# Optimization experiments

Hardware: AMD Instinct MI355X
Metric: run time of the kernel (lower is better)

The kernel has to match this reference:

```python
import jax, jax.numpy as jnp
import numpy as np
import math

EMBED_DIM = 2048
NUM_HEADS = 16
D_K = 128
BSZ = 2
SEQ = 2048


def make_freq_pos_enc(dim, max_seq_len):
    # inv_freq over dim/2 freqs, then interleave-repeat each freq twice: (f r), r=2
    inv_freq = 1.0 / (10000.0 ** (jnp.arange(0, dim, 2, dtype=jnp.float32) / dim))
    pos = jnp.arange(max_seq_len, dtype=jnp.float32)
    pe = jnp.einsum('p,f->pf', pos, inv_freq)                 # [S, dim/2]
    return jnp.repeat(pe, 2, axis=-1)                          # [S, dim], pattern (f r)


def rotate_half(u):
    # pairs are interleaved: (..., d r) with r=2
    u = u.reshape(*u.shape[:-1], -1, 2)
    u1, u2 = u[..., 0], u[..., 1]
    return jnp.stack((-u2, u1), axis=-1).reshape(*u.shape[:-2], -1)


def rotate(u, pos_enc):
    pe = pos_enc[: u.shape[-2]]                                # [S, d_k]
    return u * jnp.cos(pe) + rotate_half(u) * jnp.sin(pe)


def setup_inputs() -> dict:
    key = jax.random.key(0)
    ks = jax.random.split(key, 5)
    scale = 1.0 / math.sqrt(EMBED_DIM)
    return {
        'x': jax.random.normal(ks[0], (BSZ, SEQ, EMBED_DIM), dtype=jnp.float32),
        'wq': jax.random.normal(ks[1], (NUM_HEADS * D_K, EMBED_DIM), dtype=jnp.float32) * scale,
        'wk': jax.random.normal(ks[2], (NUM_HEADS * D_K, EMBED_DIM), dtype=jnp.float32) * scale,
        'wv': jax.random.normal(ks[3], (NUM_HEADS * D_K, EMBED_DIM), dtype=jnp.float32) * scale,
        'wo': jax.random.normal(ks[4], (EMBED_DIM, NUM_HEADS * D_K), dtype=jnp.float32) * scale,
        'freq_pos_enc': make_freq_pos_enc(D_K, SEQ),
        'mask': jnp.zeros((SEQ, SEQ), dtype=jnp.float32),  # dead arg in original forward
        'num_heads': NUM_HEADS,
        'd_k': D_K,
    }


def reference(x, wq, wk, wv, wo, freq_pos_enc, mask, num_heads, d_k):
    bsz, seq_len, _ = x.shape
    # projections (nn.Linear, no bias): x @ W^T
    def proj(w):
        p = jnp.einsum('bse,de->bsd', x, w)
        return p.reshape(bsz, seq_len, num_heads, d_k).transpose(0, 2, 1, 3)  # [B,H,S,d]
    q, k, v = proj(wq), proj(wk), proj(wv)
    q, k = rotate(q, freq_pos_enc), rotate(k, freq_pos_enc)
    # regenerated causal mask (0 on/below diagonal, -inf above)
    causal = jnp.where(
        jnp.arange(seq_len)[:, None] >= jnp.arange(seq_len)[None, :],
        0.0, -jnp.inf).astype(x.dtype)
    scores = jnp.einsum('bhsd,bhtd->bhst', q, k) / math.sqrt(d_k) + causal
    weights = jax.nn.softmax(scores, axis=-1)
    attn = jnp.einsum('bhst,bhtd->bhsd', weights, v)           # [B,H,S,d]
    attn = attn.transpose(0, 2, 1, 3).reshape(bsz, seq_len, -1)
    return jnp.einsum('bsd,ed->bse', attn, wo)


if __name__ == '__main__':
    out = reference(**setup_inputs())
    print(out.shape, out.dtype)
```

## Files before the change

kernel.cpp:

```cpp
#include <hip/hip_runtime.h>


typedef unsigned short u16;
typedef unsigned int   u32;
typedef __attribute__((ext_vector_type(4)))  float f32x4;
typedef __attribute__((ext_vector_type(16))) float f32x16;
typedef __attribute__((ext_vector_type(8)))  short short8;
typedef __attribute__((ext_vector_type(4)))  u16   u16x4;
typedef __attribute__((ext_vector_type(2)))  u16   u16x2;

#define NB   2
#define NH   16
#define SEQ  2048
#define DK   128
#define EMB  2048

__device__ __forceinline__ u16 f2bf(float f) {
    union { float f; unsigned int u; } v; v.f = f;
    unsigned int r = v.u + 0x7FFFu + ((v.u >> 16) & 1u);
    return (u16)(r >> 16);
}
__device__ __forceinline__ float bf2f(u16 h) {
    union { unsigned int u; float f; } v; v.u = ((unsigned int)h) << 16;
    return v.f;
}
__device__ __forceinline__ f32x4 mfma16(short8 a, short8 b, f32x4 c) {
    return __builtin_amdgcn_mfma_f32_16x16x32_bf16(a, b, c, 0, 0, 0);
}
__device__ __forceinline__ f32x16 mfma32(short8 a, short8 b, f32x16 c) {
    return __builtin_amdgcn_mfma_f32_32x32x16_bf16(a, b, c, 0, 0, 0);
}

#define GLDS(gsrc, ldst) __builtin_amdgcn_global_load_lds( \
    (const __attribute__((address_space(1))) void*)(gsrc), \
    (__attribute__((address_space(3))) void*)(ldst), 16, 0, 0)

__global__ __launch_bounds__(256) void cast_f32_bf16(const float* __restrict__ in,
                                                     u16* __restrict__ out, int n4) {
    int i = blockIdx.x * 256 + threadIdx.x;
    if (i >= n4) return;
    f32x4 v = ((const f32x4*)in)[i];
    u16x4 o;
    o[0] = f2bf(v[0]); o[1] = f2bf(v[1]); o[2] = f2bf(v[2]); o[3] = f2bf(v[3]);
    ((u16x4*)out)[i] = o;
}

__global__ __launch_bounds__(256) void rope_table(const float* __restrict__ freq,
                                                  float* __restrict__ ct,
                                                  float* __restrict__ st) {
    int i = blockIdx.x * 256 + threadIdx.x;
    int s = i >> 6, d2 = i & 63;
    float pe = freq[s * DK + d2 * 2];
    ct[i] = cosf(pe);
    st[i] = sinf(pe);
}

__global__ __launch_bounds__(256) void rope_apply(u16* __restrict__ Qb, u16* __restrict__ Kb,
                                                  const float* __restrict__ ct,
                                                  const float* __restrict__ st) {
    int i = blockIdx.x * 256 + threadIdx.x;
    int d2 = i & 63;
    int s  = (i >> 6) & (SEQ - 1);
    float c  = ct[(s << 6) + d2];
    float sn = st[(s << 6) + d2];
    size_t off = (size_t)i * 2;
    u16x2 q = *(const u16x2*)(Qb + off);
    float q0 = bf2f(q[0]), q1 = bf2f(q[1]);
    u16x2 qo; qo[0] = f2bf(q0 * c - q1 * sn); qo[1] = f2bf(q1 * c + q0 * sn);
    *(u16x2*)(Qb + off) = qo;
    u16x2 k = *(const u16x2*)(Kb + off);
    float k0 = bf2f(k[0]), k1 = bf2f(k[1]);
    u16x2 ko; ko[0] = f2bf(k0 * c - k1 * sn); ko[1] = f2bf(k1 * c + k0 * sn);
    *(u16x2*)(Kb + off) = ko;
}

template <int MODE>
__global__ __launch_bounds__(256) void gemm_ring(const u16* __restrict__ A,
                                                 const u16* __restrict__ B,
                                                 void* __restrict__ Cout,
                                                 int M, int N, int K) {
    __shared__ __align__(16) u16 As[3 * 4096];
    __shared__ __align__(16) u16 Bs[3 * 4096];
    const int tid  = threadIdx.x;
    const int lane = tid & 63;
    const int wid  = tid >> 6;
    const int wm   = wid >> 1, wn = wid & 1;
    const int nwgx = (int)gridDim.x;
    const int wgid = (int)blockIdx.y * nwgx + (int)blockIdx.x;
    const int cpx  = (nwgx * (int)gridDim.y) >> 3;
    const int swz  = (wgid & 7) * cpx + (wgid >> 3);
    const int m0   = (swz % nwgx) * 128, n0 = (swz / nwgx) * 128;
    const int lr   = lane & 15, lk = lane >> 4;

    const u16* Asrc = A + (size_t)(m0 + (tid >> 2)) * K + (tid & 3) * 8;
    const u16* Bsrc = B + (size_t)(n0 + (tid >> 2)) * K + (tid & 3) * 8;
    const int  dst0 = wid * 512;

    f32x4 acc[4][4] = {};
    const int NT = K >> 5;

#pragma unroll
    for (int i = 0; i < 2; ++i) {
        GLDS(Asrc + (size_t)i * 64 * K,      &As[i * 2048 + dst0]);
        GLDS(Bsrc + (size_t)i * 64 * K,      &Bs[i * 2048 + dst0]);
    }
#pragma unroll
    for (int i = 0; i < 2; ++i) {
        GLDS(Asrc + (size_t)i * 64 * K + 32, &As[4096 + i * 2048 + dst0]);
        GLDS(Bsrc + (size_t)i * 64 * K + 32, &Bs[4096 + i * 2048 + dst0]);
    }

    int buf = 0;
    for (int t = 0; t < NT; ++t) {
        if (t < NT - 1) asm volatile("s_waitcnt vmcnt(4)" ::: "memory");
        else            asm volatile("s_waitcnt vmcnt(0)" ::: "memory");
        __builtin_amdgcn_s_barrier();

        short8 af[4], bf[4];
#pragma unroll
        for (int i = 0; i < 4; ++i)
            af[i] = *(const short8*)&As[buf * 4096 + (wm * 64 + i * 16 + lr) * 32 + lk * 8];
#pragma unroll
        for (int j = 0; j < 4; ++j)
            bf[j] = *(const short8*)&Bs[buf * 4096 + (wn * 64 + j * 16 + lr) * 32 + lk * 8];

        if (t + 2 < NT) {
            int b2 = buf + 2; if (b2 >= 3) b2 -= 3;
            const u16* a2  = Asrc + (size_t)(t + 2) * 32;
            const u16* b2p = Bsrc + (size_t)(t + 2) * 32;
#pragma unroll
            for (int i = 0; i < 2; ++i) {
                GLDS(a2  + (size_t)i * 64 * K, &As[b2 * 4096 + i * 2048 + dst0]);
                GLDS(b2p + (size_t)i * 64 * K, &Bs[b2 * 4096 + i * 2048 + dst0]);
            }
        }

        __builtin_amdgcn_s_setprio(1);
#pragma unroll
        for (int i = 0; i < 4; ++i)
#pragma unroll
            for (int j = 0; j < 4; ++j)
                acc[i][j] = mfma16(af[i], bf[j], acc[i][j]);
        __builtin_amdgcn_s_setprio(0);

        buf = (buf == 2) ? 0 : buf + 1;
    }

#pragma unroll
    for (int i = 0; i < 4; ++i) {
#pragma unroll
        for (int j = 0; j < 4; ++j) {
#pragma unroll
            for (int r = 0; r < 4; ++r) {
                int m = m0 + wm * 64 + i * 16 + lk * 4 + r;
                int n = n0 + wn * 64 + j * 16 + lr;
                float v = acc[i][j][r];
                if (MODE == 0) {
                    int b = m >> 11, s = m & (SEQ - 1), h = n >> 7, d = n & (DK - 1);
                    ((u16*)Cout)[(((size_t)(b * NH + h) * SEQ + s) * DK) + d] = f2bf(v);
                } else if (MODE == 1) {
                    int h = m >> 7, d = m & (DK - 1), b = n >> 11, s = n & (SEQ - 1);
                    ((u16*)Cout)[(((size_t)(b * NH + h) * DK + d) * SEQ) + s] = f2bf(v);
                } else {
                    ((float*)Cout)[(size_t)m * N + n] = v;
                }
            }
        }
    }
}

__global__ __launch_bounds__(64, 2) void attn32(const u16* __restrict__ Q,
                                                const u16* __restrict__ K,
                                                const u16* __restrict__ VT,
                                                u16* __restrict__ O) {
    const int gid  = blockIdx.x;
    const int bh   = (gid & 7) * 4 + ((gid >> 3) & 3);
    const int qc   = 63 - (gid >> 5);
    const int l    = threadIdx.x;
    const int q32  = l & 31;
    const int half = l >> 5;
    const int q0   = qc * 32;
    const int nt   = qc + 1;

    const u16* Qg  = Q  + ((size_t)bh * SEQ + q0) * DK;
    const u16* Kg  = K  + (size_t)bh * SEQ * DK;
    const u16* VTg = VT + (size_t)bh * DK * SEQ;

    short8 qf[8];
#pragma unroll
    for (int kq = 0; kq < 8; ++kq)
        qf[kq] = *(const short8*)(Qg + q32 * DK + kq * 16 + half * 8);

    f32x16 oacc[4] = {};
    float m = -INFINITY, lsum = 0.f;

    auto loadK = [&](short8 (&kf)[8], int t) {
#pragma unroll
        for (int kq = 0; kq < 8; ++kq)
            kf[kq] = *(const short8*)(Kg + (size_t)(t * 32 + q32) * DK + kq * 16 + half * 8);
    };
    auto loadV = [&](short8 (&vf)[8], int t) {
#pragma unroll
        for (int i = 0; i < 8; ++i) {
            int dblk = i >> 1, ch = i & 1;
            vf[i] = *(const short8*)(VTg + (size_t)(dblk * 32 + q32) * SEQ
                                     + t * 32 + ch * 16 + half * 8);
        }
    };
    auto compute = [&](short8 (&kf)[8], short8 (&vf)[8], bool diag) {
        const float rs = 0.08838834764831845f;
        f32x16 sacc = {};
#pragma unroll
        for (int kq = 0; kq < 8; ++kq) sacc = mfma32(kf[kq], qf[kq], sacc);
        float tmax = -INFINITY;
#pragma unroll
        for (int r = 0; r < 16; ++r) {
            int kk = (r & 3) + 8 * (r >> 2) + 4 * half;
            float s = sacc[r] * rs;
            if (diag && kk > q32) s = -INFINITY;
            sacc[r] = s;
            tmax = fmaxf(tmax, s);
        }
        tmax = fmaxf(tmax, __shfl_xor(tmax, 32));
        if (__any(tmax - m > 8.0f)) {
            float mn = fmaxf(m, tmax);
            float sc = __expf(m - mn);
            m = mn; lsum *= sc;
#pragma unroll
            for (int d = 0; d < 4; ++d)
#pragma unroll
                for (int r = 0; r < 16; ++r) oacc[d][r] *= sc;
        }
        float tsum = 0.f;
#pragma unroll
        for (int r = 0; r < 16; ++r) { sacc[r] = __expf(sacc[r] - m); tsum += sacc[r]; }
        tsum += __shfl_xor(tsum, 32);
        lsum += tsum;
        u32 pk[8];
#pragma unroll
        for (int i = 0; i < 8; ++i)
            pk[i] = ((u32)f2bf(sacc[2 * i + 1]) << 16) | (u32)f2bf(sacc[2 * i]);
        u32 s0 = __shfl_xor((int)pk[0], 32), s1 = __shfl_xor((int)pk[1], 32);
        u32 s2 = __shfl_xor((int)pk[2], 32), s3 = __shfl_xor((int)pk[3], 32);
        u32 s4 = __shfl_xor((int)pk[4], 32), s5 = __shfl_xor((int)pk[5], 32);
        u32 s6 = __shfl_xor((int)pk[6], 32), s7 = __shfl_xor((int)pk[7], 32);
        union { u32 wd[4]; short8 s8; } P0, P1;
        P0.wd[0] = half ? s2    : pk[0];  P0.wd[1] = half ? s3    : pk[1];
        P0.wd[2] = half ? pk[2] : s0;     P0.wd[3] = half ? pk[3] : s1;
        P1.wd[0] = half ? s6    : pk[4];  P1.wd[1] = half ? s7    : pk[5];
        P1.wd[2] = half ? pk[6] : s4;     P1.wd[3] = half ? pk[7] : s5;
#pragma unroll
        for (int d = 0; d < 4; ++d) {
            oacc[d] = mfma32(vf[2 * d],     P0.s8, oacc[d]);
            oacc[d] = mfma32(vf[2 * d + 1], P1.s8, oacc[d]);
        }
    };

    short8 kA[8], kB[8], vA[8], vB[8];
    loadK(kA, 0);
    loadV(vA, 0);
    int t = 0;
    while (true) {
        if (t + 1 < nt) { loadK(kB, t + 1); loadV(vB, t + 1); }
        compute(kA, vA, t == qc);
        if (++t >= nt) break;
        if (t + 1 < nt) { loadK(kA, t + 1); loadV(vA, t + 1); }
        compute(kB, vB, t == qc);
        if (++t >= nt) break;
    }

    float inv = 1.0f / lsum;
    const int b = bh >> 4, h = bh & 15;
    u16* Og = O + ((size_t)b * SEQ + q0 + q32) * EMB + h * DK;
#pragma unroll
    for (int d = 0; d < 4; ++d)
#pragma unroll
        for (int rq = 0; rq < 4; ++rq) {
            u16x4 o4;
#pragma unroll
            for (int j = 0; j < 4; ++j) o4[j] = f2bf(oacc[d][rq * 4 + j] * inv);
            *(u16x4*)(Og + d * 32 + rq * 8 + half * 4) = o4;
        }
}

extern "C" void kernel_launch(void* const* d_in, const int* in_sizes, int n_in,
                              void* d_out, int out_size, void* d_ws, size_t ws_size,
                              hipStream_t stream) {
    const float* x    = (const float*)d_in[0];
    const float* wq   = (const float*)d_in[1];
    const float* wk   = (const float*)d_in[2];
    const float* wv   = (const float*)d_in[3];
    const float* wo   = (const float*)d_in[4];
    const float* freq = (const float*)d_in[5];

    char* ws = (char*)d_ws;
    u16*  xb  = (u16*)(ws);
    u16*  wqb = (u16*)(ws + 16777216);
    u16*  wkb = (u16*)(ws + 25165824);
    u16*  wvb = (u16*)(ws + 33554432);
    u16*  wob = (u16*)(ws + 41943040);
    u16*  Qb  = (u16*)(ws + 50331648);
    u16*  Kb  = (u16*)(ws + 67108864);
    u16*  VTb = (u16*)(ws + 83886080);
    float* ct = (float*)(ws + 100663296);
    float* st = (float*)(ws + 101187584);
    u16*  attn = xb;

    cast_f32_bf16<<<8192, 256, 0, stream>>>(x,  xb,  2097152);
    cast_f32_bf16<<<4096, 256, 0, stream>>>(wq, wqb, 1048576);
    cast_f32_bf16<<<4096, 256, 0, stream>>>(wk, wkb, 1048576);
    cast_f32_bf16<<<4096, 256, 0, stream>>>(wv, wvb, 1048576);
    cast_f32_bf16<<<4096, 256, 0, stream>>>(wo, wob, 1048576);
    rope_table<<<512, 256, 0, stream>>>(freq, ct, st);

    gemm_ring<0><<<dim3(32, 16), 256, 0, stream>>>(xb,  wqb, Qb,  4096, 2048, 2048);
    gemm_ring<0><<<dim3(32, 16), 256, 0, stream>>>(xb,  wkb, Kb,  4096, 2048, 2048);
    gemm_ring<1><<<dim3(16, 32), 256, 0, stream>>>(wvb, xb,  VTb, 2048, 4096, 2048);

    rope_apply<<<16384, 256, 0, stream>>>(Qb, Kb, ct, st);

    attn32<<<2048, 64, 0, stream>>>(Qb, Kb, VTb, attn);

    gemm_ring<3><<<dim3(32, 16), 256, 0, stream>>>(attn, wob, d_out, 4096, 2048, 2048);
}
```

Before: 340.3 us.

## Stage K/V tiles through LDS with async copies and pair causal query chunks

The attention kernel now stages K and V^T tiles into double-buffered, XOR-swizzled shared memory with direct global-to-LDS loads and explicit vmcnt waits, replacing the per-lane register double buffering. Each block handles two query chunks (63-p and p), so causal work is balanced and the grid is halved. MFMA sections are wrapped in setprio. The intent is to cut register pressure and global load latency and to balance causal work. The cost is LDS traffic and fewer blocks in flight. It relies on a GLDS helper and hand-written waitcnt counts that must match the number of loads issued.

```diff
diff --git a/kernel.cpp b/kernel.cpp
--- a/kernel.cpp
+++ b/kernel.cpp
@@ -169,118 +169,143 @@
     }
 }
 
-__global__ __launch_bounds__(64, 2) void attn32(const u16* __restrict__ Q,
-                                                const u16* __restrict__ K,
-                                                const u16* __restrict__ VT,
-                                                u16* __restrict__ O) {
+__global__ __launch_bounds__(64, 2) void attn_lds(const u16* __restrict__ Q,
+                                                  const u16* __restrict__ K,
+                                                  const u16* __restrict__ VT,
+                                                  u16* __restrict__ O) {
     const int gid  = blockIdx.x;
     const int bh   = (gid & 7) * 4 + ((gid >> 3) & 3);
-    const int qc   = 63 - (gid >> 5);
+    const int p    = gid >> 5;
     const int l    = threadIdx.x;
     const int q32  = l & 31;
     const int half = l >> 5;
-    const int q0   = qc * 32;
-    const int nt   = qc + 1;
-
-    const u16* Qg  = Q  + ((size_t)bh * SEQ + q0) * DK;
+
+    __shared__ __align__(16) u16 Ksh[2][4096];
+    __shared__ __align__(16) u16 Vsh[2][4096];
+
     const u16* Kg  = K  + (size_t)bh * SEQ * DK;
     const u16* VTg = VT + (size_t)bh * DK * SEQ;
-
-    short8 qf[8];
-#pragma unroll
-    for (int kq = 0; kq < 8; ++kq)
-        qf[kq] = *(const short8*)(Qg + q32 * DK + kq * 16 + half * 8);
-
-    f32x16 oacc[4] = {};
-    float m = -INFINITY, lsum = 0.f;
-
-    auto loadK = [&](short8 (&kf)[8], int t) {
-#pragma unroll
-        for (int kq = 0; kq < 8; ++kq)
-            kf[kq] = *(const short8*)(Kg + (size_t)(t * 32 + q32) * DK + kq * 16 + half * 8);
-    };
-    auto loadV = [&](short8 (&vf)[8], int t) {
+    const int b = bh >> 4, h = bh & 15;
+
+    auto stage = [&](int t, int bufn) {
 #pragma unroll
         for (int i = 0; i < 8; ++i) {
-            int dblk = i >> 1, ch = i & 1;
-            vf[i] = *(const short8*)(VTg + (size_t)(dblk * 32 + q32) * SEQ
-                                     + t * 32 + ch * 16 + half * 8);
+            int cid = i * 64 + l;
+            int kr = cid >> 4, kc = cid & 15;
+            GLDS(Kg + (size_t)(t * 32 + kr) * DK + ((kc ^ (kr & 7)) * 8),
+                 &Ksh[bufn][i * 512]);
+            int vr = cid >> 2, vc = cid & 3;
+            GLDS(VTg + (size_t)vr * SEQ + t * 32 + ((vc ^ ((vr >> 1) & 3)) * 8),
+                 &Vsh[bufn][i * 512]);
         }
     };
-    auto compute = [&](short8 (&kf)[8], short8 (&vf)[8], bool diag) {
-        const float rs = 0.08838834764831845f;
-        f32x16 sacc = {};
-#pragma unroll
-        for (int kq = 0; kq < 8; ++kq) sacc = mfma32(kf[kq], qf[kq], sacc);
-        float tmax = -INFINITY;
-#pragma unroll
-        for (int r = 0; r < 16; ++r) {
-            int kk = (r & 3) + 8 * (r >> 2) + 4 * half;
-            float s = sacc[r] * rs;
-            if (diag && kk > q32) s = -INFINITY;
-            sacc[r] = s;
-            tmax = fmaxf(tmax, s);
+
+    auto process = [&](int qc) {
+        const int q0 = qc * 32;
+        const int nt = qc + 1;
+        const u16* Qg = Q + ((size_t)bh * SEQ + q0) * DK;
+
+        short8 qf[8];
+#pragma unroll
+        for (int kq = 0; kq < 8; ++kq)
+            qf[kq] = *(const short8*)(Qg + q32 * DK + kq * 16 + half * 8);
+
+        f32x16 oacc[4] = {};
+        float m = -INFINITY, lsum = 0.f;
+
+        stage(0, 0);
+        for (int t = 0; t < nt; ++t) {
+            const int buf = t & 1;
+            if (t + 1 < nt) {
+                stage(t + 1, (t + 1) & 1);
+                asm volatile("s_waitcnt vmcnt(16)" ::: "memory");
+            } else {
+                asm volatile("s_waitcnt vmcnt(0)" ::: "memory");
+            }
+            __builtin_amdgcn_sched_barrier(0);
+
+            const float rs = 0.08838834764831845f;
+            short8 kf[8], vf[8];
+#pragma unroll
+            for (int kq = 0; kq < 8; ++kq) {
+                int c = (kq * 2 + half) ^ (q32 & 7);
+                kf[kq] = *(const short8*)&Ksh[buf][q32 * 128 + c * 8];
+            }
+#pragma unroll
+            for (int i = 0; i < 8; ++i) {
+                int dblk = i >> 1, ch = i & 1;
+                int vrow = dblk * 32 + q32;
+                int c = (ch * 2 + half) ^ ((q32 >> 1) & 3);
+                vf[i] = *(const short8*)&Vsh[buf][vrow * 32 + c * 8];
+            }
+            const bool diag = (t == qc);
+
+            f32x16 sacc = {};
+            __builtin_amdgcn_s_setprio(1);
+#pragma unroll
+            for (int kq = 0; kq < 8; ++kq) sacc = mfma32(kf[kq], qf[kq], sacc);
+            __builtin_amdgcn_s_setprio(0);
+            float tmax = -INFINITY;
+#pragma unroll
+            for (int r = 0; r < 16; ++r) {
+                int kk = (r & 3) + 8 * (r >> 2) + 4 * half;
+                float s = sacc[r] * rs;
+                if (diag && kk > q32) s = -INFINITY;
+                sacc[r] = s;
+                tmax = fmaxf(tmax, s);
+            }
+            tmax = fmaxf(tmax, __shfl_xor(tmax, 32));
+            if (__any(tmax - m > 8.0f)) {
+                float mn = fmaxf(m, tmax);
+                float sc = __expf(m - mn);
+                m = mn; lsum *= sc;
+#pragma unroll
+                for (int d = 0; d < 4; ++d)
+#pragma unroll
+                    for (int r = 0; r < 16; ++r) oacc[d][r] *= sc;
+            }
+            float tsum = 0.f;
+#pragma unroll
+            for (int r = 0; r < 16; ++r) { sacc[r] = __expf(sacc[r] - m); tsum += sacc[r]; }
+            tsum += __shfl_xor(tsum, 32);
+            lsum += tsum;
+            u32 pk[8];
+#pragma unroll
+            for (int i = 0; i < 8; ++i)
+                pk[i] = ((u32)f2bf(sacc[2 * i + 1]) << 16) | (u32)f2bf(sacc[2 * i]);
+            u32 s0 = __shfl_xor((int)pk[0], 32), s1 = __shfl_xor((int)pk[1], 32);
+            u32 s2 = __shfl_xor((int)pk[2], 32), s3 = __shfl_xor((int)pk[3], 32);
+            u32 s4 = __shfl_xor((int)pk[4], 32), s5 = __shfl_xor((int)pk[5], 32);
+            u32 s6 = __shfl_xor((int)pk[6], 32), s7 = __shfl_xor((int)pk[7], 32);
+            union { u32 wd[4]; short8 s8; } P0, P1;
+            P0.wd[0] = half ? s2    : pk[0];  P0.wd[1] = half ? s3    : pk[1];
+            P0.wd[2] = half ? pk[2] : s0;     P0.wd[3] = half ? pk[3] : s1;
+            P1.wd[0] = half ? s6    : pk[4];  P1.wd[1] = half ? s7    : pk[5];
+            P1.wd[2] = half ? pk[6] : s4;     P1.wd[3] = half ? pk[7] : s5;
+            __builtin_amdgcn_s_setprio(1);
+#pragma unroll
+            for (int d = 0; d < 4; ++d) {
+                oacc[d] = mfma32(vf[2 * d],     P0.s8, oacc[d]);
+                oacc[d] = mfma32(vf[2 * d + 1], P1.s8, oacc[d]);
+            }
+            __builtin_amdgcn_s_setprio(0);
         }
-        tmax = fmaxf(tmax, __shfl_xor(tmax, 32));
-        if (__any(tmax - m > 8.0f)) {
-            float mn = fmaxf(m, tmax);
-            float sc = __expf(m - mn);
-            m = mn; lsum *= sc;
-#pragma unroll
-            for (int d = 0; d < 4; ++d)
-#pragma unroll
-                for (int r = 0; r < 16; ++r) oacc[d][r] *= sc;
-        }
-        float tsum = 0.f;
-#pragma unroll
-        for (int r = 0; r < 16; ++r) { sacc[r] = __expf(sacc[r] - m); tsum += sacc[r]; }
-        tsum += __shfl_xor(tsum, 32);
-        lsum += tsum;
-        u32 pk[8];
-#pragma unroll
-        for (int i = 0; i < 8; ++i)
-            pk[i] = ((u32)f2bf(sacc[2 * i + 1]) << 16) | (u32)f2bf(sacc[2 * i]);
-        u32 s0 = __shfl_xor((int)pk[0], 32), s1 = __shfl_xor((int)pk[1], 32);
-        u32 s2 = __shfl_xor((int)pk[2], 32), s3 = __shfl_xor((int)pk[3], 32);
-        u32 s4 = __shfl_xor((int)pk[4], 32), s5 = __shfl_xor((int)pk[5], 32);
-        u32 s6 = __shfl_xor((int)pk[6], 32), s7 = __shfl_xor((int)pk[7], 32);
-        union { u32 wd[4]; short8 s8; } P0, P1;
-        P0.wd[0] = half ? s2    : pk[0];  P0.wd[1] = half ? s3    : pk[1];
-        P0.wd[2] = half ? pk[2] : s0;     P0.wd[3] = half ? pk[3] : s1;
-        P1.wd[0] = half ? s6    : pk[4];  P1.wd[1] = half ? s7    : pk[5];
-        P1.wd[2] = half ? pk[6] : s4;     P1.wd[3] = half ? pk[7] : s5;
-#pragma unroll
-        for (int d = 0; d < 4; ++d) {
-            oacc[d] = mfma32(vf[2 * d],     P0.s8, oacc[d]);
-            oacc[d] = mfma32(vf[2 * d + 1], P1.s8, oacc[d]);
-        }
+
+        float inv = 1.0f / lsum;
+        u16* Og = O + ((size_t)b * SEQ + q0 + q32) * EMB + h * DK;
+#pragma unroll
+        for (int d = 0; d < 4; ++d)
+#pragma unroll
+            for (int rq = 0; rq < 4; ++rq) {
+                u16x4 o4;
+#pragma unroll
+                for (int j = 0; j < 4; ++j) o4[j] = f2bf(oacc[d][rq * 4 + j] * inv);
+                *(u16x4*)(Og + d * 32 + rq * 8 + half * 4) = o4;
+            }
     };
 
-    short8 kA[8], kB[8], vA[8], vB[8];
-    loadK(kA, 0);
-    loadV(vA, 0);
-    int t = 0;
-    while (true) {
-        if (t + 1 < nt) { loadK(kB, t + 1); loadV(vB, t + 1); }
-        compute(kA, vA, t == qc);
-        if (++t >= nt) break;
-        if (t + 1 < nt) { loadK(kA, t + 1); loadV(vA, t + 1); }
-        compute(kB, vB, t == qc);
-        if (++t >= nt) break;
-    }
-
-    float inv = 1.0f / lsum;
-    const int b = bh >> 4, h = bh & 15;
-    u16* Og = O + ((size_t)b * SEQ + q0 + q32) * EMB + h * DK;
-#pragma unroll
-    for (int d = 0; d < 4; ++d)
-#pragma unroll
-        for (int rq = 0; rq < 4; ++rq) {
-            u16x4 o4;
-#pragma unroll
-            for (int j = 0; j < 4; ++j) o4[j] = f2bf(oacc[d][rq * 4 + j] * inv);
-            *(u16x4*)(Og + d * 32 + rq * 8 + half * 4) = o4;
-        }
+    process(63 - p);
+    process(p);
 }
 
 extern "C" void kernel_launch(void* const* d_in, const int* in_sizes, int n_in,
@@ -319,7 +344,7 @@
 
     rope_apply<<<16384, 256, 0, stream>>>(Qb, Kb, ct, st);
 
-    attn32<<<2048, 64, 0, stream>>>(Qb, Kb, VTb, attn);
+    attn_lds<<<1024, 64, 0, stream>>>(Qb, Kb, VTb, attn);
 
     gemm_ring<3><<<dim3(32, 16), 256, 0, stream>>>(attn, wob, d_out, 4096, 2048, 2048);
 }
```

Measured after the change: 305.0 us. 1.12x faster.
